# Kernel optimization log

Measured on AMD Instinct MI355X. Metric: run time of the kernel, lower is better.

Reference implementation:

```python
import jax, jax.numpy as jnp
import numpy as np

N_NODES = 100000
N_EDGES = 1600000
F_IN, F_HID, F_OUT = 256, 128, 32


def setup_inputs() -> dict:
    key = jax.random.key(0)
    k1, k2, k3, k4 = jax.random.split(key, 4)
    x = jax.random.normal(k1, (N_NODES, F_IN), dtype=jnp.float32)
    edge_index = jax.random.randint(k2, (2, N_EDGES), 0, N_NODES, dtype=jnp.int64)
    W1 = jax.random.normal(k3, (F_IN, F_HID), dtype=jnp.float32) * (1.0 / np.sqrt(F_IN))
    b1 = jnp.zeros((F_HID,), dtype=jnp.float32)
    W2 = jax.random.normal(k4, (F_HID, F_OUT), dtype=jnp.float32) * (1.0 / np.sqrt(F_HID))
    b2 = jnp.zeros((F_OUT,), dtype=jnp.float32)
    return {"x": x, "edge_index": edge_index, "W1": W1, "b1": b1, "W2": W2, "b2": b2}


def _gcn_norm(edge_index, num_nodes):
    # Add self-loops, then symmetric normalization deg^-1/2[src] * deg^-1/2[dst].
    loops = jnp.arange(num_nodes, dtype=edge_index.dtype)
    src = jnp.concatenate([edge_index[0], loops])
    dst = jnp.concatenate([edge_index[1], loops])
    deg = jax.ops.segment_sum(jnp.ones_like(dst, dtype=jnp.float32), dst,
                              num_segments=num_nodes)
    dinv = jnp.where(deg > 0, jax.lax.rsqrt(deg), 0.0)
    norm = dinv[src] * dinv[dst]  # [E + N]
    return src, dst, norm


def _gcn_conv(h, src, dst, norm, num_nodes):
    # h already linearly transformed. Gather sources, scale, scatter-add to dst.
    msgs = h[src] * norm[:, None]
    return jax.ops.segment_sum(msgs, dst, num_segments=num_nodes)


def reference(x, edge_index, W1, b1, W2, b2):
    n = x.shape[0]
    src, dst, norm = _gcn_norm(edge_index, n)
    # Layer 1: linear -> normalized scatter-add -> bias -> relu
    h = _gcn_conv(x @ W1, src, dst, norm, n) + b1
    h = jax.nn.relu(h)
    # F.dropout with training=False (eval mode) is identity.
    # Layer 2
    out = _gcn_conv(h @ W2, src, dst, norm, n) + b2
    return jax.nn.log_softmax(out, axis=1)
```

## Files before the change

### kernel.cpp

```cpp
#include <hip/hip_runtime.h>

#define N_NODES 100000
#define N_EDGES 1600000
#define F_IN 256
#define F_HID 128
#define F_OUT 32
#define NBUCK 391
#define BIN_BLOCKS 512
#define EDGES_PER_BIN 3125

typedef unsigned short ushort_t;
typedef unsigned int uint_t;

using short8  = __attribute__((ext_vector_type(8))) short;
using floatx4 = __attribute__((ext_vector_type(4))) float;

__device__ __forceinline__ ushort_t f2bf(float f) {
    uint_t u = __float_as_uint(f);
    u += 0x7fff + ((u >> 16) & 1);
    return (ushort_t)(u >> 16);
}
__device__ __forceinline__ float bf_lo(uint_t u) { return __uint_as_float(u << 16); }
__device__ __forceinline__ float bf_hi(uint_t u) { return __uint_as_float(u & 0xffff0000u); }

__global__ __launch_bounds__(256) void hist_kernel(const int* __restrict__ ei,
                                                   int* __restrict__ bucket_cnt) {
    __shared__ int h[NBUCK];
    for (int i = threadIdx.x; i < NBUCK; i += 256) h[i] = 0;
    __syncthreads();
    int gid = blockIdx.x * 256 + threadIdx.x;
    for (int e = gid; e < N_EDGES; e += BIN_BLOCKS * 256)
        atomicAdd(&h[ei[N_EDGES + e] >> 8], 1);
    __syncthreads();
    for (int i = threadIdx.x; i < NBUCK; i += 256) {
        int c = h[i];
        if (c) atomicAdd(&bucket_cnt[i], c);
    }
}

__global__ __launch_bounds__(512) void scan_kernel(const int* __restrict__ bucket_cnt,
                                                   int* __restrict__ bucket_base,
                                                   int* __restrict__ bucket_cursor,
                                                   int* __restrict__ offs) {
    __shared__ int s[512];
    int t = threadIdx.x;
    int own = (t < NBUCK) ? bucket_cnt[t] : 0;
    s[t] = own;
    __syncthreads();
    for (int off = 1; off < 512; off <<= 1) {
        int v = (t >= off) ? s[t - off] : 0;
        __syncthreads();
        s[t] += v;
        __syncthreads();
    }
    if (t < NBUCK) {
        int ex = s[t] - own;
        bucket_base[t] = ex;
        bucket_cursor[t] = ex;
    }
    if (t == 0) {
        bucket_base[NBUCK] = N_EDGES;
        offs[N_NODES] = N_EDGES;
    }
}

__global__ __launch_bounds__(256) void bin_kernel(const int* __restrict__ ei,
                                                  int* __restrict__ bucket_cursor,
                                                  int2* __restrict__ binned) {
    __shared__ int h[NBUCK];
    __shared__ int base[NBUCK];
    const int t = threadIdx.x;
    const int beg = blockIdx.x * EDGES_PER_BIN;
    const int end = beg + EDGES_PER_BIN;
    for (int i = t; i < NBUCK; i += 256) h[i] = 0;
    __syncthreads();
    for (int e = beg + t; e < end; e += 256) atomicAdd(&h[ei[N_EDGES + e] >> 8], 1);
    __syncthreads();
    for (int i = t; i < NBUCK; i += 256) {
        int c = h[i];
        base[i] = c ? atomicAdd(&bucket_cursor[i], c) : 0;
        h[i] = 0;
    }
    __syncthreads();
    for (int e = beg + t; e < end; e += 256) {
        int s = ei[e], d = ei[N_EDGES + e];
        int bk = d >> 8;
        int p = base[bk] + atomicAdd(&h[bk], 1);
        binned[p] = make_int2(s, d);
    }
}

__global__ __launch_bounds__(256) void build_kernel(const int2* __restrict__ binned,
                                                    const int* __restrict__ bucket_base,
                                                    int* __restrict__ offs,
                                                    int* __restrict__ csr,
                                                    float* __restrict__ dinv) {
    __shared__ int h[256];
    __shared__ int sc[256];
    __shared__ int cur[256];
    const int b = blockIdx.x, t = threadIdx.x;
    const int beg = bucket_base[b];
    const int end = bucket_base[b + 1];
    h[t] = 0;
    __syncthreads();
    for (int j = beg + t; j < end; j += 256) {
        int2 p = binned[j];
        atomicAdd(&h[p.y & 255], 1);
    }
    __syncthreads();
    int deg = h[t];
    sc[t] = deg;
    __syncthreads();
    for (int off = 1; off < 256; off <<= 1) {
        int v = (t >= off) ? sc[t - off] : 0;
        __syncthreads();
        sc[t] += v;
        __syncthreads();
    }
    int excl = sc[t] - deg;
    cur[t] = excl;
    int node = b * 256 + t;
    if (node < N_NODES) {
        offs[node] = beg + excl;
        dinv[node] = rsqrtf((float)deg + 1.0f);
    }
    __syncthreads();
    for (int j = beg + t; j < end; j += 256) {
        int2 p = binned[j];
        int pos = atomicAdd(&cur[p.y & 255], 1);
        csr[beg + pos] = p.x;
    }
}

__global__ __launch_bounds__(256) void wt_kernel(const float* __restrict__ W1,
                                                 const float* __restrict__ W2,
                                                 ushort_t* __restrict__ W1T,
                                                 ushort_t* __restrict__ W2T) {
    int t = blockIdx.x * 256 + threadIdx.x;
#pragma unroll
    for (int j = 0; j < 4; j++) {
        int e = j * 8192 + t;
        int n = e >> 8, k = e & 255;
        W1T[e] = f2bf(W1[k * F_HID + n]);
    }
    if (t < 4096) {
        int n = t >> 7, k = t & 127;
        W2T[t] = f2bf(W2[k * F_OUT + n]);
    }
}

__global__ __launch_bounds__(512) void gemm1_kernel(const float* __restrict__ x,
                                                    const ushort_t* __restrict__ W1T,
                                                    ushort_t* __restrict__ h0bf) {
    __shared__ ushort_t Bst[F_HID][F_IN + 8];
    const int tid = threadIdx.x;
    const int rbase = blockIdx.x * 128;
    const int w = tid >> 6;
    const int lane = tid & 63;
    const int q = lane >> 4;
    const int nloc = lane & 15;

#pragma unroll
    for (int j = 0; j < 8; j++) {
        int f = j * 512 + tid;
        int n = f >> 5, kg = f & 31;
        uint4 v = ((const uint4*)(W1T + n * F_IN))[kg];
        *(uint4*)(&Bst[n][kg * 8]) = v;
    }
    __syncthreads();

    const int rowA = rbase + w * 16 + nloc;
    const bool okA = rowA < N_NODES;
    const float* ap = x + (size_t)rowA * F_IN + q * 8;

    floatx4 acc[8];
#pragma unroll
    for (int t = 0; t < 8; t++) acc[t] = (floatx4){0.f, 0.f, 0.f, 0.f};

#pragma unroll
    for (int k0 = 0; k0 < F_IN; k0 += 32) {
        float4 f0 = make_float4(0.f, 0.f, 0.f, 0.f);
        float4 f1 = make_float4(0.f, 0.f, 0.f, 0.f);
        if (okA) {
            f0 = *(const float4*)(ap + k0);
            f1 = *(const float4*)(ap + k0 + 4);
        }
        short8 a;
        a[0] = (short)f2bf(f0.x); a[1] = (short)f2bf(f0.y);
        a[2] = (short)f2bf(f0.z); a[3] = (short)f2bf(f0.w);
        a[4] = (short)f2bf(f1.x); a[5] = (short)f2bf(f1.y);
        a[6] = (short)f2bf(f1.z); a[7] = (short)f2bf(f1.w);
#pragma unroll
        for (int t = 0; t < 8; t++) {
            short8 b = *(const short8*)(&Bst[t * 16 + nloc][k0 + q * 8]);
            acc[t] = __builtin_amdgcn_mfma_f32_16x16x32_bf16(a, b, acc[t], 0, 0, 0);
        }
    }

#pragma unroll
    for (int reg = 0; reg < 4; reg++) {
        int rowD = rbase + w * 16 + q * 4 + reg;
        if (rowD < N_NODES) {
            ushort_t* op = h0bf + (size_t)rowD * F_HID + nloc;
#pragma unroll
            for (int t = 0; t < 8; t++) op[t * 16] = f2bf(acc[t][reg]);
        }
    }
}

__global__ __launch_bounds__(256) void gather128(const ushort_t* __restrict__ h0bf,
                                                 const int* __restrict__ offs,
                                                 const int* __restrict__ csr,
                                                 const float* __restrict__ dinv,
                                                 ushort_t* __restrict__ aggbf) {
    int node = blockIdx.x * 8 + (threadIdx.x >> 5);
    int l = threadIdx.x & 31;
    float dn = dinv[node];
    uint2 sv = ((const uint2*)(h0bf + (size_t)node * F_HID))[l];
    float s = dn * dn;
    float4 acc;
    acc.x = bf_lo(sv.x) * s; acc.y = bf_hi(sv.x) * s;
    acc.z = bf_lo(sv.y) * s; acc.w = bf_hi(sv.y) * s;

    int beg = offs[node], end = offs[node + 1];
    int j = beg;
    for (; j + 3 < end; j += 4) {
        int s0 = csr[j], s1 = csr[j + 1], s2 = csr[j + 2], s3 = csr[j + 3];
        float n0 = dinv[s0] * dn, n1 = dinv[s1] * dn;
        float n2 = dinv[s2] * dn, n3 = dinv[s3] * dn;
        uint2 v0 = ((const uint2*)(h0bf + (size_t)s0 * F_HID))[l];
        uint2 v1 = ((const uint2*)(h0bf + (size_t)s1 * F_HID))[l];
        uint2 v2 = ((const uint2*)(h0bf + (size_t)s2 * F_HID))[l];
        uint2 v3 = ((const uint2*)(h0bf + (size_t)s3 * F_HID))[l];
        acc.x += bf_lo(v0.x) * n0 + bf_lo(v1.x) * n1 + bf_lo(v2.x) * n2 + bf_lo(v3.x) * n3;
        acc.y += bf_hi(v0.x) * n0 + bf_hi(v1.x) * n1 + bf_hi(v2.x) * n2 + bf_hi(v3.x) * n3;
        acc.z += bf_lo(v0.y) * n0 + bf_lo(v1.y) * n1 + bf_lo(v2.y) * n2 + bf_lo(v3.y) * n3;
        acc.w += bf_hi(v0.y) * n0 + bf_hi(v1.y) * n1 + bf_hi(v2.y) * n2 + bf_hi(v3.y) * n3;
    }
    for (; j < end; j++) {
        int s0 = csr[j];
        float n0 = dinv[s0] * dn;
        uint2 v0 = ((const uint2*)(h0bf + (size_t)s0 * F_HID))[l];
        acc.x += bf_lo(v0.x) * n0; acc.y += bf_hi(v0.x) * n0;
        acc.z += bf_lo(v0.y) * n0; acc.w += bf_hi(v0.y) * n0;
    }
    uint2 p;
    p.x = (uint_t)f2bf(acc.x) | ((uint_t)f2bf(acc.y) << 16);
    p.y = (uint_t)f2bf(acc.z) | ((uint_t)f2bf(acc.w) << 16);
    ((uint2*)(aggbf + (size_t)node * F_HID))[l] = p;
}

__global__ __launch_bounds__(256) void gemm2_kernel(const ushort_t* __restrict__ aggbf,
                                                    const float* __restrict__ b1,
                                                    const ushort_t* __restrict__ W2T,
                                                    ushort_t* __restrict__ h2bf) {
    __shared__ ushort_t Bs[F_OUT][F_HID + 8];
    __shared__ float b1s[F_HID];
    const int tid = threadIdx.x;
    const int rbase = blockIdx.x * 64;
    const int w = tid >> 6;
    const int lane = tid & 63;
    const int q = lane >> 4;
    const int nloc = lane & 15;

    if (tid < F_HID) b1s[tid] = b1[tid];
#pragma unroll
    for (int jj = 0; jj < 2; jj++) {
        int f = jj * 256 + tid;
        int n = f >> 4, kg = f & 15;
        uint4 v = ((const uint4*)(W2T + n * F_HID))[kg];
        *(uint4*)(&Bs[n][kg * 8]) = v;
    }
    __syncthreads();

    const int rowA = rbase + w * 16 + nloc;
    const bool okA = rowA < N_NODES;

    floatx4 acc[2];
    acc[0] = (floatx4){0.f, 0.f, 0.f, 0.f};
    acc[1] = (floatx4){0.f, 0.f, 0.f, 0.f};

#pragma unroll
    for (int k0 = 0; k0 < F_HID; k0 += 32) {
        int kk = k0 + q * 8;
        uint4 av = make_uint4(0, 0, 0, 0);
        if (okA) av = *(const uint4*)(aggbf + (size_t)rowA * F_HID + kk);
        float4 bb0 = *(const float4*)(&b1s[kk]);
        float4 bb1 = *(const float4*)(&b1s[kk + 4]);
        short8 a;
        a[0] = (short)f2bf(fmaxf(bf_lo(av.x) + bb0.x, 0.f));
        a[1] = (short)f2bf(fmaxf(bf_hi(av.x) + bb0.y, 0.f));
        a[2] = (short)f2bf(fmaxf(bf_lo(av.y) + bb0.z, 0.f));
        a[3] = (short)f2bf(fmaxf(bf_hi(av.y) + bb0.w, 0.f));
        a[4] = (short)f2bf(fmaxf(bf_lo(av.z) + bb1.x, 0.f));
        a[5] = (short)f2bf(fmaxf(bf_hi(av.z) + bb1.y, 0.f));
        a[6] = (short)f2bf(fmaxf(bf_lo(av.w) + bb1.z, 0.f));
        a[7] = (short)f2bf(fmaxf(bf_hi(av.w) + bb1.w, 0.f));
#pragma unroll
        for (int t = 0; t < 2; t++) {
            short8 b = *(const short8*)(&Bs[t * 16 + nloc][kk]);
            acc[t] = __builtin_amdgcn_mfma_f32_16x16x32_bf16(a, b, acc[t], 0, 0, 0);
        }
    }
#pragma unroll
    for (int reg = 0; reg < 4; reg++) {
        int rowD = rbase + w * 16 + q * 4 + reg;
        if (rowD < N_NODES) {
            ushort_t* op = h2bf + (size_t)rowD * F_OUT + nloc;
            op[0]  = f2bf(acc[0][reg]);
            op[16] = f2bf(acc[1][reg]);
        }
    }
}

__global__ __launch_bounds__(256) void gather32_lsm(const ushort_t* __restrict__ h2bf,
                                                    const int* __restrict__ offs,
                                                    const int* __restrict__ csr,
                                                    const float* __restrict__ dinv,
                                                    const float* __restrict__ b2,
                                                    float* __restrict__ out) {
    int node = blockIdx.x * 32 + (threadIdx.x >> 3);
    int l = threadIdx.x & 7;
    float dn = dinv[node];
    uint2 sv = ((const uint2*)(h2bf + (size_t)node * F_OUT))[l];
    float s = dn * dn;
    float4 acc;
    acc.x = bf_lo(sv.x) * s; acc.y = bf_hi(sv.x) * s;
    acc.z = bf_lo(sv.y) * s; acc.w = bf_hi(sv.y) * s;

    int beg = offs[node], end = offs[node + 1];
    int j = beg;
    for (; j + 3 < end; j += 4) {
        int s0 = csr[j], s1 = csr[j + 1], s2 = csr[j + 2], s3 = csr[j + 3];
        float n0 = dinv[s0] * dn, n1 = dinv[s1] * dn;
        float n2 = dinv[s2] * dn, n3 = dinv[s3] * dn;
        uint2 v0 = ((const uint2*)(h2bf + (size_t)s0 * F_OUT))[l];
        uint2 v1 = ((const uint2*)(h2bf + (size_t)s1 * F_OUT))[l];
        uint2 v2 = ((const uint2*)(h2bf + (size_t)s2 * F_OUT))[l];
        uint2 v3 = ((const uint2*)(h2bf + (size_t)s3 * F_OUT))[l];
        acc.x += bf_lo(v0.x) * n0 + bf_lo(v1.x) * n1 + bf_lo(v2.x) * n2 + bf_lo(v3.x) * n3;
        acc.y += bf_hi(v0.x) * n0 + bf_hi(v1.x) * n1 + bf_hi(v2.x) * n2 + bf_hi(v3.x) * n3;
        acc.z += bf_lo(v0.y) * n0 + bf_lo(v1.y) * n1 + bf_lo(v2.y) * n2 + bf_lo(v3.y) * n3;
        acc.w += bf_hi(v0.y) * n0 + bf_hi(v1.y) * n1 + bf_hi(v2.y) * n2 + bf_hi(v3.y) * n3;
    }
    for (; j < end; j++) {
        int s0 = csr[j];
        float n0 = dinv[s0] * dn;
        uint2 v0 = ((const uint2*)(h2bf + (size_t)s0 * F_OUT))[l];
        acc.x += bf_lo(v0.x) * n0; acc.y += bf_hi(v0.x) * n0;
        acc.z += bf_lo(v0.y) * n0; acc.w += bf_hi(v0.y) * n0;
    }
    float4 bb = ((const float4*)b2)[l];
    acc.x += bb.x; acc.y += bb.y; acc.z += bb.z; acc.w += bb.w;

    float m = fmaxf(fmaxf(acc.x, acc.y), fmaxf(acc.z, acc.w));
#pragma unroll
    for (int off = 1; off < 8; off <<= 1) m = fmaxf(m, __shfl_xor(m, off, 8));
    float es = __expf(acc.x - m) + __expf(acc.y - m) + __expf(acc.z - m) + __expf(acc.w - m);
#pragma unroll
    for (int off = 1; off < 8; off <<= 1) es += __shfl_xor(es, off, 8);
    float lse = m + __logf(es);
    float4 o = make_float4(acc.x - lse, acc.y - lse, acc.z - lse, acc.w - lse);
    ((float4*)(out + (size_t)node * F_OUT))[l] = o;
}

extern "C" void kernel_launch(void* const* d_in, const int* in_sizes, int n_in,
                              void* d_out, int out_size, void* d_ws, size_t ws_size,
                              hipStream_t stream) {
    const float* x  = (const float*)d_in[0];
    const int*   ei = (const int*)d_in[1];
    const float* W1 = (const float*)d_in[2];
    const float* b1 = (const float*)d_in[3];
    const float* W2 = (const float*)d_in[4];
    const float* b2 = (const float*)d_in[5];
    float* out = (float*)d_out;

    float* ws = (float*)d_ws;
    float*    dinv          = ws;
    int*      offs          = (int*)(ws + 100096);
    int*      bucket_cnt    = (int*)(ws + 200224);
    int*      bucket_base   = (int*)(ws + 200736);
    int*      bucket_cursor = (int*)(ws + 201248);
    int*      csr           = (int*)(ws + 201760);
    ushort_t* W1T           = (ushort_t*)(ws + 1801760);
    ushort_t* W2T           = (ushort_t*)(ws + 1818144);
    ushort_t* h0bf          = (ushort_t*)(ws + 1820192);
    ushort_t* aggbf         = (ushort_t*)(ws + 8220192);
    ushort_t* h2bf          = (ushort_t*)(ws + 14620192);
    int2*     binned        = (int2*)aggbf;

    hipMemsetAsync(bucket_cnt, 0, 512 * sizeof(int), stream);
    hist_kernel<<<BIN_BLOCKS, 256, 0, stream>>>(ei, bucket_cnt);
    scan_kernel<<<1, 512, 0, stream>>>(bucket_cnt, bucket_base, bucket_cursor, offs);
    bin_kernel<<<BIN_BLOCKS, 256, 0, stream>>>(ei, bucket_cursor, binned);
    build_kernel<<<NBUCK, 256, 0, stream>>>(binned, bucket_base, offs, csr, dinv);
    wt_kernel<<<32, 256, 0, stream>>>(W1, W2, W1T, W2T);
    gemm1_kernel<<<(N_NODES + 127) / 128, 512, 0, stream>>>(x, W1T, h0bf);
    gather128<<<N_NODES / 8, 256, 0, stream>>>(h0bf, offs, csr, dinv, aggbf);
    gemm2_kernel<<<(N_NODES + 63) / 64, 256, 0, stream>>>(aggbf, b1, W2T, h2bf);
    gather32_lsm<<<N_NODES / 32, 256, 0, stream>>>(h2bf, offs, csr, dinv, b2, out);
}
```

Measured before the change: 354.0 us.

## Fuse layer-1 gather with second GEMM and merge weight transpose into histogram

The 128-wide neighbor aggregation now happens inside the second GEMM kernel. Each block gathers 64 nodes, applies bias and ReLU, stores the bf16 rows in shared memory, then runs the MFMA product against W2. This removes the round trip of the aggregated activation through global memory and one kernel launch. The weight transpose/convert kernel is also folded into extra blocks of the histogram kernel, saving another launch. The trade-off is fewer, larger blocks for the gather phase (64 nodes per block, 8 sequential per half-warp), which may reduce parallelism and latency hiding in the memory-bound gather.

```diff
diff --git a/kernel.cpp b/kernel.cpp
--- a/kernel.cpp
+++ b/kernel.cpp
@@ -23,18 +23,36 @@
 __device__ __forceinline__ float bf_lo(uint_t u) { return __uint_as_float(u << 16); }
 __device__ __forceinline__ float bf_hi(uint_t u) { return __uint_as_float(u & 0xffff0000u); }
 
-__global__ __launch_bounds__(256) void hist_kernel(const int* __restrict__ ei,
-                                                   int* __restrict__ bucket_cnt) {
+__global__ __launch_bounds__(256) void histwt_kernel(const int* __restrict__ ei,
+                                                     int* __restrict__ bucket_cnt,
+                                                     const float* __restrict__ W1,
+                                                     const float* __restrict__ W2,
+                                                     ushort_t* __restrict__ W1T,
+                                                     ushort_t* __restrict__ W2T) {
     __shared__ int h[NBUCK];
-    for (int i = threadIdx.x; i < NBUCK; i += 256) h[i] = 0;
-    __syncthreads();
-    int gid = blockIdx.x * 256 + threadIdx.x;
-    for (int e = gid; e < N_EDGES; e += BIN_BLOCKS * 256)
-        atomicAdd(&h[ei[N_EDGES + e] >> 8], 1);
-    __syncthreads();
-    for (int i = threadIdx.x; i < NBUCK; i += 256) {
-        int c = h[i];
-        if (c) atomicAdd(&bucket_cnt[i], c);
+    if (blockIdx.x < BIN_BLOCKS) {
+        for (int i = threadIdx.x; i < NBUCK; i += 256) h[i] = 0;
+        __syncthreads();
+        int gid = blockIdx.x * 256 + threadIdx.x;
+        for (int e = gid; e < N_EDGES; e += BIN_BLOCKS * 256)
+            atomicAdd(&h[ei[N_EDGES + e] >> 8], 1);
+        __syncthreads();
+        for (int i = threadIdx.x; i < NBUCK; i += 256) {
+            int c = h[i];
+            if (c) atomicAdd(&bucket_cnt[i], c);
+        }
+    } else {
+        int t = (blockIdx.x - BIN_BLOCKS) * 256 + threadIdx.x;
+#pragma unroll
+        for (int j = 0; j < 4; j++) {
+            int e = j * 8192 + t;
+            int n = e >> 8, k = e & 255;
+            W1T[e] = f2bf(W1[k * F_HID + n]);
+        }
+        if (t < 4096) {
+            int n = t >> 7, k = t & 127;
+            W2T[t] = f2bf(W2[k * F_OUT + n]);
+        }
     }
 }
 
@@ -132,23 +150,6 @@
     }
 }
 
-__global__ __launch_bounds__(256) void wt_kernel(const float* __restrict__ W1,
-                                                 const float* __restrict__ W2,
-                                                 ushort_t* __restrict__ W1T,
-                                                 ushort_t* __restrict__ W2T) {
-    int t = blockIdx.x * 256 + threadIdx.x;
-#pragma unroll
-    for (int j = 0; j < 4; j++) {
-        int e = j * 8192 + t;
-        int n = e >> 8, k = e & 255;
-        W1T[e] = f2bf(W1[k * F_HID + n]);
-    }
-    if (t < 4096) {
-        int n = t >> 7, k = t & 127;
-        W2T[t] = f2bf(W2[k * F_OUT + n]);
-    }
-}
-
 __global__ __launch_bounds__(512) void gemm1_kernel(const float* __restrict__ x,
                                                     const ushort_t* __restrict__ W1T,
                                                     ushort_t* __restrict__ h0bf) {
@@ -208,62 +209,18 @@
     }
 }
 
-__global__ __launch_bounds__(256) void gather128(const ushort_t* __restrict__ h0bf,
-                                                 const int* __restrict__ offs,
-                                                 const int* __restrict__ csr,
-                                                 const float* __restrict__ dinv,
-                                                 ushort_t* __restrict__ aggbf) {
-    int node = blockIdx.x * 8 + (threadIdx.x >> 5);
-    int l = threadIdx.x & 31;
-    float dn = dinv[node];
-    uint2 sv = ((const uint2*)(h0bf + (size_t)node * F_HID))[l];
-    float s = dn * dn;
-    float4 acc;
-    acc.x = bf_lo(sv.x) * s; acc.y = bf_hi(sv.x) * s;
-    acc.z = bf_lo(sv.y) * s; acc.w = bf_hi(sv.y) * s;
-
-    int beg = offs[node], end = offs[node + 1];
-    int j = beg;
-    for (; j + 3 < end; j += 4) {
-        int s0 = csr[j], s1 = csr[j + 1], s2 = csr[j + 2], s3 = csr[j + 3];
-        float n0 = dinv[s0] * dn, n1 = dinv[s1] * dn;
-        float n2 = dinv[s2] * dn, n3 = dinv[s3] * dn;
-        uint2 v0 = ((const uint2*)(h0bf + (size_t)s0 * F_HID))[l];
-        uint2 v1 = ((const uint2*)(h0bf + (size_t)s1 * F_HID))[l];
-        uint2 v2 = ((const uint2*)(h0bf + (size_t)s2 * F_HID))[l];
-        uint2 v3 = ((const uint2*)(h0bf + (size_t)s3 * F_HID))[l];
-        acc.x += bf_lo(v0.x) * n0 + bf_lo(v1.x) * n1 + bf_lo(v2.x) * n2 + bf_lo(v3.x) * n3;
-        acc.y += bf_hi(v0.x) * n0 + bf_hi(v1.x) * n1 + bf_hi(v2.x) * n2 + bf_hi(v3.x) * n3;
-        acc.z += bf_lo(v0.y) * n0 + bf_lo(v1.y) * n1 + bf_lo(v2.y) * n2 + bf_lo(v3.y) * n3;
-        acc.w += bf_hi(v0.y) * n0 + bf_hi(v1.y) * n1 + bf_hi(v2.y) * n2 + bf_hi(v3.y) * n3;
-    }
-    for (; j < end; j++) {
-        int s0 = csr[j];
-        float n0 = dinv[s0] * dn;
-        uint2 v0 = ((const uint2*)(h0bf + (size_t)s0 * F_HID))[l];
-        acc.x += bf_lo(v0.x) * n0; acc.y += bf_hi(v0.x) * n0;
-        acc.z += bf_lo(v0.y) * n0; acc.w += bf_hi(v0.y) * n0;
-    }
-    uint2 p;
-    p.x = (uint_t)f2bf(acc.x) | ((uint_t)f2bf(acc.y) << 16);
-    p.y = (uint_t)f2bf(acc.z) | ((uint_t)f2bf(acc.w) << 16);
-    ((uint2*)(aggbf + (size_t)node * F_HID))[l] = p;
-}
-
-__global__ __launch_bounds__(256) void gemm2_kernel(const ushort_t* __restrict__ aggbf,
-                                                    const float* __restrict__ b1,
-                                                    const ushort_t* __restrict__ W2T,
-                                                    ushort_t* __restrict__ h2bf) {
+__global__ __launch_bounds__(256) void gg2_kernel(const ushort_t* __restrict__ h0bf,
+                                                  const int* __restrict__ offs,
+                                                  const int* __restrict__ csr,
+                                                  const float* __restrict__ dinv,
+                                                  const float* __restrict__ b1,
+                                                  const ushort_t* __restrict__ W2T,
+                                                  ushort_t* __restrict__ h2bf) {
+    __shared__ ushort_t As[64][F_HID + 8];
     __shared__ ushort_t Bs[F_OUT][F_HID + 8];
-    __shared__ float b1s[F_HID];
     const int tid = threadIdx.x;
     const int rbase = blockIdx.x * 64;
-    const int w = tid >> 6;
-    const int lane = tid & 63;
-    const int q = lane >> 4;
-    const int nloc = lane & 15;
-
-    if (tid < F_HID) b1s[tid] = b1[tid];
+
 #pragma unroll
     for (int jj = 0; jj < 2; jj++) {
         int f = jj * 256 + tid;
@@ -271,35 +228,70 @@
         uint4 v = ((const uint4*)(W2T + n * F_HID))[kg];
         *(uint4*)(&Bs[n][kg * 8]) = v;
     }
-    __syncthreads();
-
-    const int rowA = rbase + w * 16 + nloc;
-    const bool okA = rowA < N_NODES;
-
-    floatx4 acc[2];
-    acc[0] = (floatx4){0.f, 0.f, 0.f, 0.f};
-    acc[1] = (floatx4){0.f, 0.f, 0.f, 0.f};
+
+    const int hw = tid >> 5;
+    const int l = tid & 31;
+    const float4 b1v = *(const float4*)(b1 + l * 4);
+
+    for (int u = 0; u < 8; u++) {
+        int node = rbase + hw * 8 + u;
+        float4 acc = make_float4(0.f, 0.f, 0.f, 0.f);
+        if (node < N_NODES) {
+            float dn = dinv[node];
+            uint2 sv = ((const uint2*)(h0bf + (size_t)node * F_HID))[l];
+            float s = dn * dn;
+            acc.x = bf_lo(sv.x) * s; acc.y = bf_hi(sv.x) * s;
+            acc.z = bf_lo(sv.y) * s; acc.w = bf_hi(sv.y) * s;
+
+            int beg = offs[node], end = offs[node + 1];
+            int j = beg;
+            for (; j + 3 < end; j += 4) {
+                int s0 = csr[j], s1 = csr[j + 1], s2 = csr[j + 2], s3 = csr[j + 3];
+                float n0 = dinv[s0] * dn, n1 = dinv[s1] * dn;
+                float n2 = dinv[s2] * dn, n3 = dinv[s3] * dn;
+                uint2 v0 = ((const uint2*)(h0bf + (size_t)s0 * F_HID))[l];
+                uint2 v1 = ((const uint2*)(h0bf + (size_t)s1 * F_HID))[l];
+                uint2 v2 = ((const uint2*)(h0bf + (size_t)s2 * F_HID))[l];
+                uint2 v3 = ((const uint2*)(h0bf + (size_t)s3 * F_HID))[l];
+                acc.x += bf_lo(v0.x) * n0 + bf_lo(v1.x) * n1 + bf_lo(v2.x) * n2 + bf_lo(v3.x) * n3;
+                acc.y += bf_hi(v0.x) * n0 + bf_hi(v1.x) * n1 + bf_hi(v2.x) * n2 + bf_hi(v3.x) * n3;
+                acc.z += bf_lo(v0.y) * n0 + bf_lo(v1.y) * n1 + bf_lo(v2.y) * n2 + bf_lo(v3.y) * n3;
+                acc.w += bf_hi(v0.y) * n0 + bf_hi(v1.y) * n1 + bf_hi(v2.y) * n2 + bf_hi(v3.y) * n3;
+            }
+            for (; j < end; j++) {
+                int s0 = csr[j];
+                float n0 = dinv[s0] * dn;
+                uint2 v0 = ((const uint2*)(h0bf + (size_t)s0 * F_HID))[l];
+                acc.x += bf_lo(v0.x) * n0; acc.y += bf_hi(v0.x) * n0;
+                acc.z += bf_lo(v0.y) * n0; acc.w += bf_hi(v0.y) * n0;
+            }
+        }
+        uint2 p;
+        p.x = (uint_t)f2bf(fmaxf(acc.x + b1v.x, 0.f)) |
+              ((uint_t)f2bf(fmaxf(acc.y + b1v.y, 0.f)) << 16);
+        p.y = (uint_t)f2bf(fmaxf(acc.z + b1v.z, 0.f)) |
+              ((uint_t)f2bf(fmaxf(acc.w + b1v.w, 0.f)) << 16);
+        *(uint2*)(&As[hw * 8 + u][l * 4]) = p;
+    }
+    __syncthreads();
+
+    const int w = tid >> 6;
+    const int lane = tid & 63;
+    const int q = lane >> 4;
+    const int nloc = lane & 15;
+
+    floatx4 acc2[2];
+    acc2[0] = (floatx4){0.f, 0.f, 0.f, 0.f};
+    acc2[1] = (floatx4){0.f, 0.f, 0.f, 0.f};
 
 #pragma unroll
     for (int k0 = 0; k0 < F_HID; k0 += 32) {
         int kk = k0 + q * 8;
-        uint4 av = make_uint4(0, 0, 0, 0);
-        if (okA) av = *(const uint4*)(aggbf + (size_t)rowA * F_HID + kk);
-        float4 bb0 = *(const float4*)(&b1s[kk]);
-        float4 bb1 = *(const float4*)(&b1s[kk + 4]);
-        short8 a;
-        a[0] = (short)f2bf(fmaxf(bf_lo(av.x) + bb0.x, 0.f));
-        a[1] = (short)f2bf(fmaxf(bf_hi(av.x) + bb0.y, 0.f));
-        a[2] = (short)f2bf(fmaxf(bf_lo(av.y) + bb0.z, 0.f));
-        a[3] = (short)f2bf(fmaxf(bf_hi(av.y) + bb0.w, 0.f));
-        a[4] = (short)f2bf(fmaxf(bf_lo(av.z) + bb1.x, 0.f));
-        a[5] = (short)f2bf(fmaxf(bf_hi(av.z) + bb1.y, 0.f));
-        a[6] = (short)f2bf(fmaxf(bf_lo(av.w) + bb1.z, 0.f));
-        a[7] = (short)f2bf(fmaxf(bf_hi(av.w) + bb1.w, 0.f));
+        short8 a = *(const short8*)(&As[w * 16 + nloc][kk]);
 #pragma unroll
         for (int t = 0; t < 2; t++) {
             short8 b = *(const short8*)(&Bs[t * 16 + nloc][kk]);
-            acc[t] = __builtin_amdgcn_mfma_f32_16x16x32_bf16(a, b, acc[t], 0, 0, 0);
+            acc2[t] = __builtin_amdgcn_mfma_f32_16x16x32_bf16(a, b, acc2[t], 0, 0, 0);
         }
     }
 #pragma unroll
@@ -307,8 +299,8 @@
         int rowD = rbase + w * 16 + q * 4 + reg;
         if (rowD < N_NODES) {
             ushort_t* op = h2bf + (size_t)rowD * F_OUT + nloc;
-            op[0]  = f2bf(acc[0][reg]);
-            op[16] = f2bf(acc[1][reg]);
+            op[0]  = f2bf(acc2[0][reg]);
+            op[16] = f2bf(acc2[1][reg]);
         }
     }
 }
@@ -385,18 +377,15 @@
     ushort_t* W1T           = (ushort_t*)(ws + 1801760);
     ushort_t* W2T           = (ushort_t*)(ws + 1818144);
     ushort_t* h0bf          = (ushort_t*)(ws + 1820192);
-    ushort_t* aggbf         = (ushort_t*)(ws + 8220192);
+    int2*     binned        = (int2*)(ws + 8220192);
     ushort_t* h2bf          = (ushort_t*)(ws + 14620192);
-    int2*     binned        = (int2*)aggbf;
 
     hipMemsetAsync(bucket_cnt, 0, 512 * sizeof(int), stream);
-    hist_kernel<<<BIN_BLOCKS, 256, 0, stream>>>(ei, bucket_cnt);
+    histwt_kernel<<<BIN_BLOCKS + 32, 256, 0, stream>>>(ei, bucket_cnt, W1, W2, W1T, W2T);
     scan_kernel<<<1, 512, 0, stream>>>(bucket_cnt, bucket_base, bucket_cursor, offs);
     bin_kernel<<<BIN_BLOCKS, 256, 0, stream>>>(ei, bucket_cursor, binned);
     build_kernel<<<NBUCK, 256, 0, stream>>>(binned, bucket_base, offs, csr, dinv);
-    wt_kernel<<<32, 256, 0, stream>>>(W1, W2, W1T, W2T);
     gemm1_kernel<<<(N_NODES + 127) / 128, 512, 0, stream>>>(x, W1T, h0bf);
-    gather128<<<N_NODES / 8, 256, 0, stream>>>(h0bf, offs, csr, dinv, aggbf);
-    gemm2_kernel<<<(N_NODES + 63) / 64, 256, 0, stream>>>(aggbf, b1, W2T, h2bf);
+    gg2_kernel<<<(N_NODES + 63) / 64, 256, 0, stream>>>(h0bf, offs, csr, dinv, b1, W2T, h2bf);
     gather32_lsm<<<N_NODES / 32, 256, 0, stream>>>(h2bf, offs, csr, dinv, b2, out);
 }
```

Result: slower. 376.7 us (+6.4%).
